# Kernel tuning notes

Hardware: AMD Instinct MI355X
Metric: run time of the kernel (lower is better)

The kernel has to match this reference:

```python
import jax, jax.numpy as jnp
import numpy as np

N = 50000
E = 1600000
D = 128
H = 16  # SE hidden = int(128 * 0.125)
EPS = 1e-5


def _layernorm(x, gamma, beta):
    mu = jnp.mean(x, axis=-1, keepdims=True)
    var = jnp.mean(jnp.square(x - mu), axis=-1, keepdims=True)
    return (x - mu) * jax.lax.rsqrt(var + EPS) * gamma + beta


def _gcn_conv(x, W, b, src, dst):
    # PyG GCNConv, improved=True: self-loop weight 2.0, symmetric norm.
    xw = x @ W                                        # [N, D]
    deg = jax.ops.segment_sum(jnp.ones((E,), x.dtype), dst, num_segments=N) + 2.0
    dinv = jnp.where(deg > 0, jax.lax.rsqrt(deg), 0.0)  # [N]
    norm = dinv[src] * dinv[dst]                      # [E]
    agg = jax.ops.segment_sum(xw[src] * norm[:, None], dst, num_segments=N)
    agg = agg + xw * (2.0 * dinv * dinv)[:, None]     # self-loop contribution
    return agg + b


def setup_inputs() -> dict:
    key = jax.random.key(0)
    ks = jax.random.split(key, 10)
    scale = 1.0 / np.sqrt(D)
    inp = {
        "x": jax.random.normal(ks[0], (N, D), jnp.float32),
        "edge_index": jax.random.randint(ks[1], (2, E), 0, N, jnp.int64),
        "W1": jax.random.normal(ks[2], (D, D), jnp.float32) * scale,
        "b1": jnp.zeros((D,), jnp.float32),
        "g1": jnp.ones((D,), jnp.float32),
        "beta1": jnp.zeros((D,), jnp.float32),
        "W2": jax.random.normal(ks[3], (D, D), jnp.float32) * scale,
        "b2": jnp.zeros((D,), jnp.float32),
        "g2": jnp.ones((D,), jnp.float32),
        "beta2": jnp.zeros((D,), jnp.float32),
        "Ws": jax.random.normal(ks[4], (D, H), jnp.float32) * scale,
        "bs": jnp.zeros((H,), jnp.float32),
        "We": jax.random.normal(ks[5], (H, D), jnp.float32) * (1.0 / np.sqrt(H)),
        "be": jnp.zeros((D,), jnp.float32),
    }
    return inp


def reference(x, edge_index, W1, b1, g1, beta1, W2, b2, g2, beta2, Ws, bs, We, be):
    src, dst = edge_index[0], edge_index[1]
    skip = x
    h = jax.nn.relu(_layernorm(_gcn_conv(x, W1, b1, src, dst), g1, beta1))
    h = _layernorm(_gcn_conv(h, W2, b2, src, dst), g2, beta2)
    # SE gating
    s = jax.nn.relu(h @ Ws + bs)
    w = jax.nn.sigmoid(s @ We + be)
    h = h * w
    return jax.nn.relu(h + skip)
```

## Files before the change

### kernel.cpp

```cpp
#include <hip/hip_runtime.h>
#include <math.h>

#define DD 128
#define HH 16
#define NB 256
#define TILE 8192
#define SEGCAP 24576
#define EPSV 1e-5f

typedef unsigned long long u64;
typedef __attribute__((ext_vector_type(8))) short short8;
typedef __attribute__((ext_vector_type(4))) float f32x4;
union U4S8 { uint4 u; short8 s; };

static __device__ __forceinline__ ushort f2bf(float f) {
  uint u = __float_as_uint(f);
  u += 0x7FFFu + ((u >> 16) & 1u);
  return (ushort)(u >> 16);
}
static __device__ __forceinline__ float bflo(uint u) { return __uint_as_float(u << 16); }
static __device__ __forceinline__ float bfhi(uint u) { return __uint_as_float(u & 0xFFFF0000u); }


__global__ void k_hist_cvt(const int* __restrict__ dst, int* __restrict__ deg, int ecnt,
                           const float2* __restrict__ x2, uint* __restrict__ xb,
                           int ncnt) {
  int stride = gridDim.x * blockDim.x;
  int t0 = blockIdx.x * blockDim.x + threadIdx.x;
  for (int e = t0; e < ecnt; e += stride) atomicAdd(&deg[dst[e]], 1);
  for (int k = t0; k < ncnt; k += stride) {
    float2 v = x2[k];
    xb[k] = (uint)f2bf(v.x) | ((uint)f2bf(v.y) << 16);
  }
}


#define SCAN_T 1024
#define SCAN_I 4

__global__ void k_scan1(const int* __restrict__ deg, u64* __restrict__ bsum, int n) {
  __shared__ u64 sh[SCAN_T];
  int tid = threadIdx.x;
  int base = blockIdx.x * SCAN_T * SCAN_I + tid * SCAN_I;
  u64 s = 0;
#pragma unroll
  for (int j = 0; j < SCAN_I; ++j) {
    int i = base + j;
    if (i < n) {
      int d = deg[i];
      int dp = (d + 7) & ~7;
      s += ((u64)dp << 32) | (u64)(uint)d;
    }
  }
  sh[tid] = s;
  __syncthreads();
  for (int off = SCAN_T / 2; off > 0; off >>= 1) {
    if (tid < off) sh[tid] += sh[tid + off];
    __syncthreads();
  }
  if (tid == 0) bsum[blockIdx.x] = sh[0];
}

__global__ void k_scan2(const int* __restrict__ deg, const u64* __restrict__ bsum,
                        int* __restrict__ rowoff, int* __restrict__ cursor,
                        int* __restrict__ bucketBase, int* __restrict__ bucketCur,
                        int n) {
  __shared__ u64 sh[SCAN_T];
  __shared__ u64 sbase;
  int tid = threadIdx.x;
  int b = blockIdx.x;
  if (tid == 0) { u64 s = 0; for (int j = 0; j < b; ++j) s += bsum[j]; sbase = s; }
  int base = b * SCAN_T * SCAN_I + tid * SCAN_I;
  int d[SCAN_I]; u64 ts = 0;
#pragma unroll
  for (int j = 0; j < SCAN_I; ++j) {
    int i = base + j;
    d[j] = (i < n) ? deg[i] : 0;
    int dp = (d[j] + 7) & ~7;
    ts += ((u64)dp << 32) | (u64)(uint)d[j];
  }
  sh[tid] = ts;
  __syncthreads();
  for (int off = 1; off < SCAN_T; off <<= 1) {
    u64 v = (tid >= off) ? sh[tid - off] : 0;
    __syncthreads();
    sh[tid] += v;
    __syncthreads();
  }
  u64 ex = sbase + sh[tid] - ts;
#pragma unroll
  for (int j = 0; j < SCAN_I; ++j) {
    int i = base + j;
    if (i < n) {
      int ro = (int)(ex >> 32);
      int raw = (int)(ex & 0xFFFFFFFFu);
      rowoff[i] = ro;
      cursor[i] = ro;
      int bq = (int)(((uint)i * NB) / (uint)n);
      if (i == (bq * n + NB - 1) / NB) { bucketBase[bq] = raw; bucketCur[bq] = raw; }
      int dp = (d[j] + 7) & ~7;
      ex += ((u64)dp << 32) | (u64)(uint)d[j];
      if (i == n - 1) rowoff[n] = (int)(ex >> 32);
    }
  }
}


static __device__ __forceinline__ void gemm_mfma_body(
    const uint4* __restrict__ A16, const float* __restrict__ B,
    const int* __restrict__ deg, ushort* __restrict__ C, int nrows, int bx) {
  int tid = threadIdx.x;
  int wv = tid >> 6, l = tid & 63;
  int rowbase = (bx >> 1) * 64;
  int c0 = (bx & 1) * 64;
  int colb = c0 + (wv << 4) + (l & 15);
  int kb = (l >> 4) << 3;
  uint4 bf[4];
#pragma unroll
  for (int ks = 0; ks < 4; ++ks) {
    const float* Bp = B + (size_t)(ks * 32 + kb) * DD + colb;
    float b0 = Bp[0], b1 = Bp[DD], b2 = Bp[2 * DD], b3 = Bp[3 * DD];
    float b4 = Bp[4 * DD], b5 = Bp[5 * DD], b6 = Bp[6 * DD], b7 = Bp[7 * DD];
    bf[ks].x = (uint)f2bf(b0) | ((uint)f2bf(b1) << 16);
    bf[ks].y = (uint)f2bf(b2) | ((uint)f2bf(b3) << 16);
    bf[ks].z = (uint)f2bf(b4) | ((uint)f2bf(b5) << 16);
    bf[ks].w = (uint)f2bf(b6) | ((uint)f2bf(b7) << 16);
  }
#pragma unroll
  for (int rt = 0; rt < 4; ++rt) {
    int r = rowbase + rt * 16 + (l & 15);
    int rc = (r < nrows) ? r : (nrows - 1);
    f32x4 acc = {0.f, 0.f, 0.f, 0.f};
#pragma unroll
    for (int ks = 0; ks < 4; ++ks) {
      U4S8 ua, ub;
      ua.u = A16[(size_t)rc * 16 + (ks << 2) + (l >> 4)];
      ub.u = bf[ks];
      acc = __builtin_amdgcn_mfma_f32_16x16x32_bf16(ua.s, ub.s, acc, 0, 0, 0);
    }
#pragma unroll
    for (int ri = 0; ri < 4; ++ri) {
      int row = rowbase + rt * 16 + ((l >> 4) << 2) + ri;
      if (row < nrows) {
        float dv = rsqrtf((float)deg[row] + 2.0f);
        C[(size_t)row * DD + colb] = f2bf(acc[ri] * dv);
      }
    }
  }
}


__global__ __launch_bounds__(256) void k_gemm1_bucket(
    const uint4* __restrict__ A16, const float* __restrict__ B,
    const int* __restrict__ deg, ushort* __restrict__ C, int nrows,
    const int* __restrict__ src, const int* __restrict__ dst,
    int* __restrict__ bucketCur, uint* __restrict__ pairs, int ecnt,
    int abloks, int gblocks) {
  __shared__ uint smem[8960];
  int bx = blockIdx.x;
  if (bx >= abloks) {
    gemm_mfma_body(A16, B, deg, C, nrows, bx - abloks);
    return;
  }
  uint* stag  = smem;
  uint* cnt   = smem + 8192;
  uint* gbase = smem + 8448;
  uint* cur   = smem + 8704;
  int tid = threadIdx.x;
  int ntiles = (ecnt + TILE - 1) / TILE;
  for (int t = bx; t < ntiles; t += abloks) {
    int base = t * TILE;
    int cntE = min(TILE, ecnt - base);
    cnt[tid] = 0;
    __syncthreads();
    for (int k = tid; k < cntE; k += 256) {
      uint d = (uint)dst[base + k];
      atomicAdd(&cnt[(d * NB) / (uint)nrows], 1u);
    }
    __syncthreads();
    uint myc = cnt[tid];
    uint gb = atomicAdd((uint*)&bucketCur[tid], myc);
    uint v = myc;
#pragma unroll
    for (int off = 1; off < 64; off <<= 1) {
      uint u = __shfl_up(v, off, 64);
      if ((tid & 63) >= off) v += u;
    }
    if ((tid & 63) == 63) gbase[tid >> 6] = v;
    __syncthreads();
    uint add = 0;
#pragma unroll
    for (int wvi = 0; wvi < 4; ++wvi) add += (wvi < (tid >> 6)) ? gbase[wvi] : 0;
    uint excl = add + v - myc;
    __syncthreads();
    cnt[tid] = excl;
    gbase[tid] = gb;
    cur[tid] = 0;
    __syncthreads();
    for (int k = tid; k < cntE; k += 256) {
      uint d = (uint)dst[base + k];
      uint s = (uint)src[base + k];
      uint b = (d * NB) / (uint)nrows;
      uint li = atomicAdd(&cur[b], 1u);
      stag[cnt[b] + li] = (d << 16) | s;
    }
    __syncthreads();
    int wv = tid >> 6, ln = tid & 63;
    for (int b = wv; b < 256; b += 4) {
      uint c = cur[b], o = cnt[b], g = gbase[b];
      for (uint k2 = (uint)ln; k2 < c; k2 += 64) pairs[g + k2] = stag[o + k2];
    }
    __syncthreads();
  }
}

__global__ __launch_bounds__(256) void k_gemmb(
    const uint4* __restrict__ A16, const float* __restrict__ B,
    const int* __restrict__ deg, ushort* __restrict__ C, int nrows) {
  gemm_mfma_body(A16, B, deg, C, nrows, blockIdx.x);
}


__global__ __launch_bounds__(256) void k_csrb(
    const uint* __restrict__ pairs, const int* __restrict__ bucketBase,
    const int* __restrict__ rowoff, const int* __restrict__ deg,
    int* __restrict__ cursor, ushort* __restrict__ csr, int n, int ecnt) {
  __shared__ ushort seg[SEGCAP];
  __shared__ int curs[256];
  int b = blockIdx.x;
  int tid = threadIdx.x;
  int d0 = (b * n + NB - 1) / NB;
  int d1 = ((b + 1) * n + NB - 1) / NB;
  int segbase = rowoff[d0];
  int seglen = rowoff[d1] - segbase;
  int pbase = bucketBase[b];
  int pend = (b == NB - 1) ? ecnt : bucketBase[b + 1];
  if (seglen <= SEGCAP) {
    for (int dl = tid; dl < d1 - d0; dl += 256) curs[dl] = rowoff[d0 + dl] - segbase;
    __syncthreads();
    for (int p = pbase + tid; p < pend; p += 256) {
      uint pr = pairs[p];
      int pos = atomicAdd(&curs[(int)(pr >> 16) - d0], 1);
      seg[pos] = (ushort)(pr & 0xFFFFu);
    }
    __syncthreads();
    for (int dl = tid; dl < d1 - d0; dl += 256) {
      int e0 = curs[dl], e1 = rowoff[d0 + dl + 1] - segbase;
      for (int k = e0; k < e1; ++k) seg[k] = (ushort)n;
    }
    __syncthreads();
    uint4* outp4 = (uint4*)(csr + segbase);
    const uint4* sp = (const uint4*)seg;
    int nq = seglen >> 3;
    for (int k = tid; k < nq; k += 256) outp4[k] = sp[k];
  } else {
    for (int p = pbase + tid; p < pend; p += 256) {
      uint pr = pairs[p];
      int pos = atomicAdd(&cursor[pr >> 16], 1);
      csr[pos] = (ushort)(pr & 0xFFFFu);
    }
    __syncthreads();
    for (int dl = tid; dl < d1 - d0; dl += 256) {
      int d = d0 + dl;
      for (int k = rowoff[d] + deg[d]; k < rowoff[d + 1]; ++k) csr[k] = (ushort)n;
    }
  }
}


static __device__ __forceinline__ void edge_accum(
    const uint* __restrict__ xw32, const ushort* __restrict__ csr,
    int start, int cnt, uint lane, float& acc0, float& acc1) {
  const uint4* cs = (const uint4*)(csr + __builtin_amdgcn_readfirstlane(start));
  int rem = __builtin_amdgcn_readfirstlane(cnt);
  uint4 c;
  if (rem >= 8) c = *cs++;
  while (rem >= 16) {
    uint v[8];
    v[0] = xw32[((c.x & 0xFFFFu) << 6) + lane];
    v[1] = xw32[((c.x >> 16) << 6) + lane];
    v[2] = xw32[((c.y & 0xFFFFu) << 6) + lane];
    v[3] = xw32[((c.y >> 16) << 6) + lane];
    v[4] = xw32[((c.z & 0xFFFFu) << 6) + lane];
    v[5] = xw32[((c.z >> 16) << 6) + lane];
    v[6] = xw32[((c.w & 0xFFFFu) << 6) + lane];
    v[7] = xw32[((c.w >> 16) << 6) + lane];
    uint4 cn = *cs++;
#pragma unroll
    for (int j = 0; j < 8; ++j) {
      acc0 += bflo(v[j]);
      acc1 += bfhi(v[j]);
    }
    c = cn; rem -= 8;
  }
  if (rem >= 8) {
    uint v[8];
    v[0] = xw32[((c.x & 0xFFFFu) << 6) + lane];
    v[1] = xw32[((c.x >> 16) << 6) + lane];
    v[2] = xw32[((c.y & 0xFFFFu) << 6) + lane];
    v[3] = xw32[((c.y >> 16) << 6) + lane];
    v[4] = xw32[((c.z & 0xFFFFu) << 6) + lane];
    v[5] = xw32[((c.z >> 16) << 6) + lane];
    v[6] = xw32[((c.w & 0xFFFFu) << 6) + lane];
    v[7] = xw32[((c.w >> 16) << 6) + lane];
#pragma unroll
    for (int j = 0; j < 8; ++j) {
      acc0 += bflo(v[j]);
      acc1 += bfhi(v[j]);
    }
  }
}


__global__ __launch_bounds__(256) void k_agg1(
    const ushort* __restrict__ xwd, const ushort* __restrict__ csr,
    const int* __restrict__ rowoff, const int* __restrict__ deg,
    const float* __restrict__ bias, const float* __restrict__ gam,
    const float* __restrict__ bet, uint* __restrict__ outp, int n) {
  int wv = threadIdx.x >> 6, lane = threadIdx.x & 63;
  int i = blockIdx.x * 4 + wv;
  if (i >= n) return;
  int start = rowoff[i], cnt = rowoff[i + 1] - start;
  float di = rsqrtf((float)deg[i] + 2.0f);
  const uint* xw32 = (const uint*)xwd;
  float acc0 = 0.f, acc1 = 0.f;
  edge_accum(xw32, csr, start, cnt, (uint)lane, acc0, acc1);
  uint su = xw32[((uint)i << 6) + lane];
  float2 bv = ((const float2*)bias)[lane];
  float c0v = fmaf(di, acc0 + 2.f * bflo(su), bv.x);
  float c1v = fmaf(di, acc1 + 2.f * bfhi(su), bv.y);
  float s = c0v + c1v;
#pragma unroll
  for (int off = 32; off > 0; off >>= 1) s += __shfl_xor(s, off);
  float mu = s * (1.f / DD);
  float c0 = c0v - mu, c1 = c1v - mu;
  float q = c0 * c0 + c1 * c1;
#pragma unroll
  for (int off = 32; off > 0; off >>= 1) q += __shfl_xor(q, off);
  float rstd = rsqrtf(q * (1.f / DD) + EPSV);
  float2 gv = ((const float2*)gam)[lane];
  float2 tv = ((const float2*)bet)[lane];
  float h0 = fmaxf(fmaf(c0 * rstd, gv.x, tv.x), 0.f);
  float h1 = fmaxf(fmaf(c1 * rstd, gv.y, tv.y), 0.f);
  uint packed = (uint)f2bf(h0) | ((uint)f2bf(h1) << 16);
  __builtin_nontemporal_store(packed, &outp[((uint)i << 6) + lane]);
}


__global__ __launch_bounds__(256) void k_agg2(
    const ushort* __restrict__ xwd, const ushort* __restrict__ csr,
    const int* __restrict__ rowoff, const int* __restrict__ deg,
    const float* __restrict__ bias, const float* __restrict__ gam,
    const float* __restrict__ bet, const float* __restrict__ Ws,
    const float* __restrict__ bs, const float* __restrict__ We,
    const float* __restrict__ be, const float* __restrict__ xin,
    float* __restrict__ outp, int n) {
  int wv = threadIdx.x >> 6, lane = threadIdx.x & 63;
  int i = blockIdx.x * 4 + wv;
  if (i >= n) return;
  int start = rowoff[i], cnt = rowoff[i + 1] - start;
  float di = rsqrtf((float)deg[i] + 2.0f);
  const uint* xw32 = (const uint*)xwd;
  float acc0 = 0.f, acc1 = 0.f;
  edge_accum(xw32, csr, start, cnt, (uint)lane, acc0, acc1);
  uint su = xw32[((uint)i << 6) + lane];
  float2 bv = ((const float2*)bias)[lane];
  float c0v = fmaf(di, acc0 + 2.f * bflo(su), bv.x);
  float c1v = fmaf(di, acc1 + 2.f * bfhi(su), bv.y);
  float s = c0v + c1v;
#pragma unroll
  for (int off = 32; off > 0; off >>= 1) s += __shfl_xor(s, off);
  float mu = s * (1.f / DD);
  float c0 = c0v - mu, c1 = c1v - mu;
  float q = c0 * c0 + c1 * c1;
#pragma unroll
  for (int off = 32; off > 0; off >>= 1) q += __shfl_xor(q, off);
  float rstd = rsqrtf(q * (1.f / DD) + EPSV);
  float2 gv = ((const float2*)gam)[lane];
  float2 tv = ((const float2*)bet)[lane];
  float h0 = fmaf(c0 * rstd, gv.x, tv.x);
  float h1 = fmaf(c1 * rstd, gv.y, tv.y);
  float pj[HH];
  const float* wr0 = &Ws[(2 * lane) * HH];
  const float* wr1 = &Ws[(2 * lane + 1) * HH];
#pragma unroll
  for (int j = 0; j < HH; ++j) pj[j] = h0 * wr0[j] + h1 * wr1[j];
#pragma unroll
  for (int off = 32; off > 0; off >>= 1) {
#pragma unroll
    for (int j = 0; j < HH; ++j) pj[j] += __shfl_xor(pj[j], off);
  }
  float2 bev = ((const float2*)be)[lane];
  float wacc0 = bev.x, wacc1 = bev.y;
#pragma unroll
  for (int j = 0; j < HH; ++j) {
    float sj = fmaxf(pj[j] + bs[j], 0.f);
    float2 wev = ((const float2*)(We + j * DD))[lane];
    wacc0 = fmaf(sj, wev.x, wacc0);
    wacc1 = fmaf(sj, wev.y, wacc1);
  }
  float w0 = 1.f / (1.f + __expf(-wacc0));
  float w1 = 1.f / (1.f + __expf(-wacc1));
  float2 xr = ((const float2*)(xin + (size_t)i * DD))[lane];
  float2 o;
  o.x = fmaxf(fmaf(h0, w0, xr.x), 0.f);
  o.y = fmaxf(fmaf(h1, w1, xr.y), 0.f);
  ((float2*)(outp + (size_t)i * DD))[lane] = o;
}


extern "C" void kernel_launch(void* const* d_in, const int* in_sizes, int n_in,
                              void* d_out, int out_size, void* d_ws, size_t ws_size,
                              hipStream_t stream) {
  const float* x   = (const float*)d_in[0];
  const int*   ei  = (const int*)d_in[1];
  const float* W1  = (const float*)d_in[2];
  const float* b1  = (const float*)d_in[3];
  const float* g1  = (const float*)d_in[4];
  const float* be1 = (const float*)d_in[5];
  const float* W2  = (const float*)d_in[6];
  const float* b2  = (const float*)d_in[7];
  const float* g2  = (const float*)d_in[8];
  const float* be2 = (const float*)d_in[9];
  const float* Ws  = (const float*)d_in[10];
  const float* bs  = (const float*)d_in[11];
  const float* We  = (const float*)d_in[12];
  const float* bee = (const float*)d_in[13];
  float* outp = (float*)d_out;

  int n    = in_sizes[0] / DD;
  int ecnt = in_sizes[1] / 2;
  const int* src = ei;
  const int* dst = ei + ecnt;

  size_t maxent = (size_t)ecnt + 8 * (size_t)n + 64;

  char* w = (char*)d_ws;
  ushort* xwd    = (ushort*)w; w += (size_t)(n + 1) * DD * 2;
  uint*   h1     = (uint*)w;   w += (size_t)n * DD * 2;
  uint*   xb     = (uint*)w;   w += (size_t)n * DD * 2;
  int*    deg    = (int*)w;    w += (size_t)n * 4;
  int*    cursor = (int*)w;    w += (size_t)n * 4;
  int*    rowoff = (int*)w;    w += (size_t)(n + 1) * 4;
  w = (char*)(((size_t)w + 7) & ~(size_t)7);
  u64*    bsum   = (u64*)w;    w += 64 * 8;
  int*    bktB   = (int*)w;    w += NB * 4;
  int*    bktC   = (int*)w;    w += NB * 4;
  w = (char*)(((size_t)w + 15) & ~(size_t)15);
  uint*   pairs  = (uint*)w;   w += ((size_t)ecnt + 64) * 4;
  w = (char*)(((size_t)w + 15) & ~(size_t)15);
  ushort* csr    = (ushort*)w; w += maxent * 2;

  hipMemsetAsync(deg, 0, (size_t)n * 4, stream);
  hipMemsetAsync(xwd + (size_t)n * DD, 0, DD * 2, stream);

  const int TB = 256;
  k_hist_cvt<<<2048, TB, 0, stream>>>(dst, deg, ecnt, (const float2*)x, xb, n * 64);
  int nb = (n + SCAN_T * SCAN_I - 1) / (SCAN_T * SCAN_I);
  k_scan1<<<nb, SCAN_T, 0, stream>>>(deg, bsum, n);
  k_scan2<<<nb, SCAN_T, 0, stream>>>(deg, bsum, rowoff, cursor, bktB, bktC, n);

  int gblocks = ((n + 63) / 64) * 2;
  int abloks = (ecnt + TILE - 1) / TILE;
  k_gemm1_bucket<<<abloks + gblocks, TB, 0, stream>>>(
      (const uint4*)xb, W1, deg, xwd, n, src, dst, bktC, pairs, ecnt, abloks, gblocks);
  k_csrb<<<NB, TB, 0, stream>>>(pairs, bktB, rowoff, deg, cursor, csr, n, ecnt);

  int nb4 = (n + 3) / 4;
  k_agg1<<<nb4, TB, 0, stream>>>(xwd, csr, rowoff, deg, b1, g1, be1, h1, n);
  k_gemmb<<<gblocks, TB, 0, stream>>>((const uint4*)h1, W2, deg, xwd, n);
  k_agg2<<<nb4, TB, 0, stream>>>(xwd, csr, rowoff, deg, b2, g2, be2,
                                 Ws, bs, We, bee, x, outp, n);
}
```

Measured before the change: 310.9 us.

## Fuse second GEMM into first aggregation and pre-pack weights into MFMA fragments

The layer-1 aggregation kernel now keeps each block's four normalized rows in shared memory as bf16. It multiplies them by a pre-packed W2 with MFMA and writes the scaled second-layer features directly. This removes the h1 intermediate buffer's store and reload and the separate second GEMM launch. The first GEMM now reads fp32 x and converts to bf16 inline, which drops the standalone x conversion pass. Both weight matrices are packed once into MFMA fragment layout inside the histogram kernel. In exchange, the fused MFMA uses only 4 of its 16 rows, so most of that compute is wasted, and it adds a block-wide barrier.

```diff
diff --git a/kernel.cpp b/kernel.cpp
--- a/kernel.cpp
+++ b/kernel.cpp
@@ -18,19 +18,32 @@
   u += 0x7FFFu + ((u >> 16) & 1u);
   return (ushort)(u >> 16);
 }
+static __device__ __forceinline__ uint pk(float a, float b) {
+  return (uint)f2bf(a) | ((uint)f2bf(b) << 16);
+}
 static __device__ __forceinline__ float bflo(uint u) { return __uint_as_float(u << 16); }
 static __device__ __forceinline__ float bfhi(uint u) { return __uint_as_float(u & 0xFFFF0000u); }
 
 
-__global__ void k_hist_cvt(const int* __restrict__ dst, int* __restrict__ deg, int ecnt,
-                           const float2* __restrict__ x2, uint* __restrict__ xb,
-                           int ncnt) {
+__global__ void k_hist_prep(const int* __restrict__ dst, int* __restrict__ deg, int ecnt,
+                            const float* __restrict__ W1, const float* __restrict__ W2,
+                            uint4* __restrict__ W1f, uint4* __restrict__ W2f) {
   int stride = gridDim.x * blockDim.x;
   int t0 = blockIdx.x * blockDim.x + threadIdx.x;
   for (int e = t0; e < ecnt; e += stride) atomicAdd(&deg[dst[e]], 1);
-  for (int k = t0; k < ncnt; k += stride) {
-    float2 v = x2[k];
-    xb[k] = (uint)f2bf(v.x) | ((uint)f2bf(v.y) << 16);
+  for (int t = t0; t < 4096; t += stride) {
+    int m = t >> 11;
+    int r = t & 2047;
+    int ct = r >> 8, ks = (r >> 6) & 3, l = r & 63;
+    int col = ct * 16 + (l & 15);
+    int kb = ks * 32 + ((l >> 4) << 3);
+    const float* W = m ? W2 : W1;
+    uint4 v;
+    v.x = pk(W[(kb + 0) * DD + col], W[(kb + 1) * DD + col]);
+    v.y = pk(W[(kb + 2) * DD + col], W[(kb + 3) * DD + col]);
+    v.z = pk(W[(kb + 4) * DD + col], W[(kb + 5) * DD + col]);
+    v.w = pk(W[(kb + 6) * DD + col], W[(kb + 7) * DD + col]);
+    (m ? W2f : W1f)[(ct * 4 + ks) * 64 + l] = v;
   }
 }
 
@@ -106,26 +119,17 @@
 }
 
 
-static __device__ __forceinline__ void gemm_mfma_body(
-    const uint4* __restrict__ A16, const float* __restrict__ B,
+static __device__ __forceinline__ void gemm_mfma_x(
+    const float* __restrict__ x, const uint4* __restrict__ W1f,
     const int* __restrict__ deg, ushort* __restrict__ C, int nrows, int bx) {
   int tid = threadIdx.x;
   int wv = tid >> 6, l = tid & 63;
   int rowbase = (bx >> 1) * 64;
-  int c0 = (bx & 1) * 64;
-  int colb = c0 + (wv << 4) + (l & 15);
-  int kb = (l >> 4) << 3;
+  int ctg = (bx & 1) * 4 + wv;
+  int colb = ctg * 16 + (l & 15);
   uint4 bf[4];
 #pragma unroll
-  for (int ks = 0; ks < 4; ++ks) {
-    const float* Bp = B + (size_t)(ks * 32 + kb) * DD + colb;
-    float b0 = Bp[0], b1 = Bp[DD], b2 = Bp[2 * DD], b3 = Bp[3 * DD];
-    float b4 = Bp[4 * DD], b5 = Bp[5 * DD], b6 = Bp[6 * DD], b7 = Bp[7 * DD];
-    bf[ks].x = (uint)f2bf(b0) | ((uint)f2bf(b1) << 16);
-    bf[ks].y = (uint)f2bf(b2) | ((uint)f2bf(b3) << 16);
-    bf[ks].z = (uint)f2bf(b4) | ((uint)f2bf(b5) << 16);
-    bf[ks].w = (uint)f2bf(b6) | ((uint)f2bf(b7) << 16);
-  }
+  for (int ks = 0; ks < 4; ++ks) bf[ks] = W1f[(ctg * 4 + ks) * 64 + l];
 #pragma unroll
   for (int rt = 0; rt < 4; ++rt) {
     int r = rowbase + rt * 16 + (l & 15);
@@ -133,8 +137,13 @@
     f32x4 acc = {0.f, 0.f, 0.f, 0.f};
 #pragma unroll
     for (int ks = 0; ks < 4; ++ks) {
+      const float4* xp = (const float4*)(x + (size_t)rc * DD + ks * 32 + ((l >> 4) << 3));
+      float4 a0 = xp[0], a1 = xp[1];
       U4S8 ua, ub;
-      ua.u = A16[(size_t)rc * 16 + (ks << 2) + (l >> 4)];
+      ua.u.x = pk(a0.x, a0.y);
+      ua.u.y = pk(a0.z, a0.w);
+      ua.u.z = pk(a1.x, a1.y);
+      ua.u.w = pk(a1.z, a1.w);
       ub.u = bf[ks];
       acc = __builtin_amdgcn_mfma_f32_16x16x32_bf16(ua.s, ub.s, acc, 0, 0, 0);
     }
@@ -151,7 +160,7 @@
 
 
 __global__ __launch_bounds__(256) void k_gemm1_bucket(
-    const uint4* __restrict__ A16, const float* __restrict__ B,
+    const float* __restrict__ x, const uint4* __restrict__ W1f,
     const int* __restrict__ deg, ushort* __restrict__ C, int nrows,
     const int* __restrict__ src, const int* __restrict__ dst,
     int* __restrict__ bucketCur, uint* __restrict__ pairs, int ecnt,
@@ -159,7 +168,7 @@
   __shared__ uint smem[8960];
   int bx = blockIdx.x;
   if (bx >= abloks) {
-    gemm_mfma_body(A16, B, deg, C, nrows, bx - abloks);
+    gemm_mfma_x(x, W1f, deg, C, nrows, bx - abloks);
     return;
   }
   uint* stag  = smem;
@@ -212,12 +221,6 @@
     }
     __syncthreads();
   }
-}
-
-__global__ __launch_bounds__(256) void k_gemmb(
-    const uint4* __restrict__ A16, const float* __restrict__ B,
-    const int* __restrict__ deg, ushort* __restrict__ C, int nrows) {
-  gemm_mfma_body(A16, B, deg, C, nrows, blockIdx.x);
 }
 
 
@@ -312,20 +315,23 @@
 }
 
 
-__global__ __launch_bounds__(256) void k_agg1(
+__global__ __launch_bounds__(256) void k_agg1f(
     const ushort* __restrict__ xwd, const ushort* __restrict__ csr,
     const int* __restrict__ rowoff, const int* __restrict__ deg,
     const float* __restrict__ bias, const float* __restrict__ gam,
-    const float* __restrict__ bet, uint* __restrict__ outp, int n) {
+    const float* __restrict__ bet, const uint4* __restrict__ W2f,
+    ushort* __restrict__ xwd2, int n) {
+  __shared__ uint hls[16 * 64];
+  __shared__ float dvs[4];
   int wv = threadIdx.x >> 6, lane = threadIdx.x & 63;
   int i = blockIdx.x * 4 + wv;
-  if (i >= n) return;
-  int start = rowoff[i], cnt = rowoff[i + 1] - start;
-  float di = rsqrtf((float)deg[i] + 2.0f);
+  int iv = (i < n) ? i : (n - 1);
+  int start = rowoff[iv], cnt = rowoff[iv + 1] - start;
+  float di = rsqrtf((float)deg[iv] + 2.0f);
   const uint* xw32 = (const uint*)xwd;
   float acc0 = 0.f, acc1 = 0.f;
   edge_accum(xw32, csr, start, cnt, (uint)lane, acc0, acc1);
-  uint su = xw32[((uint)i << 6) + lane];
+  uint su = xw32[((uint)iv << 6) + lane];
   float2 bv = ((const float2*)bias)[lane];
   float c0v = fmaf(di, acc0 + 2.f * bflo(su), bv.x);
   float c1v = fmaf(di, acc1 + 2.f * bfhi(su), bv.y);
@@ -342,8 +348,29 @@
   float2 tv = ((const float2*)bet)[lane];
   float h0 = fmaxf(fmaf(c0 * rstd, gv.x, tv.x), 0.f);
   float h1 = fmaxf(fmaf(c1 * rstd, gv.y, tv.y), 0.f);
-  uint packed = (uint)f2bf(h0) | ((uint)f2bf(h1) << 16);
-  __builtin_nontemporal_store(packed, &outp[((uint)i << 6) + lane]);
+  hls[wv * 64 + lane] = pk(h0, h1);
+  if (lane == 0) dvs[wv] = di;
+  __syncthreads();
+#pragma unroll
+  for (int cti = 0; cti < 2; ++cti) {
+    int ct = wv * 2 + cti;
+    f32x4 acc = {0.f, 0.f, 0.f, 0.f};
+#pragma unroll
+    for (int ks = 0; ks < 4; ++ks) {
+      U4S8 ua, ub;
+      ua.u = *(const uint4*)&hls[(lane & 15) * 64 + ks * 16 + ((lane >> 4) << 2)];
+      ub.u = W2f[(ct * 4 + ks) * 64 + lane];
+      acc = __builtin_amdgcn_mfma_f32_16x16x32_bf16(ua.s, ub.s, acc, 0, 0, 0);
+    }
+    if (lane < 16) {
+#pragma unroll
+      for (int ri = 0; ri < 4; ++ri) {
+        int node = blockIdx.x * 4 + ri;
+        if (node < n)
+          xwd2[(size_t)node * DD + ct * 16 + lane] = f2bf(acc[ri] * dvs[ri]);
+      }
+    }
+  }
 }
 
 
@@ -437,12 +464,13 @@
 
   char* w = (char*)d_ws;
   ushort* xwd    = (ushort*)w; w += (size_t)(n + 1) * DD * 2;
-  uint*   h1     = (uint*)w;   w += (size_t)n * DD * 2;
-  uint*   xb     = (uint*)w;   w += (size_t)n * DD * 2;
+  ushort* xwd2   = (ushort*)w; w += (size_t)(n + 1) * DD * 2;
   int*    deg    = (int*)w;    w += (size_t)n * 4;
   int*    cursor = (int*)w;    w += (size_t)n * 4;
   int*    rowoff = (int*)w;    w += (size_t)(n + 1) * 4;
-  w = (char*)(((size_t)w + 7) & ~(size_t)7);
+  w = (char*)(((size_t)w + 15) & ~(size_t)15);
+  uint4*  W1f    = (uint4*)w;  w += 2048 * 16;
+  uint4*  W2f    = (uint4*)w;  w += 2048 * 16;
   u64*    bsum   = (u64*)w;    w += 64 * 8;
   int*    bktB   = (int*)w;    w += NB * 4;
   int*    bktC   = (int*)w;    w += NB * 4;
@@ -453,9 +481,10 @@
 
   hipMemsetAsync(deg, 0, (size_t)n * 4, stream);
   hipMemsetAsync(xwd + (size_t)n * DD, 0, DD * 2, stream);
+  hipMemsetAsync(xwd2 + (size_t)n * DD, 0, DD * 2, stream);
 
   const int TB = 256;
-  k_hist_cvt<<<2048, TB, 0, stream>>>(dst, deg, ecnt, (const float2*)x, xb, n * 64);
+  k_hist_prep<<<2048, TB, 0, stream>>>(dst, deg, ecnt, W1, W2, W1f, W2f);
   int nb = (n + SCAN_T * SCAN_I - 1) / (SCAN_T * SCAN_I);
   k_scan1<<<nb, SCAN_T, 0, stream>>>(deg, bsum, n);
   k_scan2<<<nb, SCAN_T, 0, stream>>>(deg, bsum, rowoff, cursor, bktB, bktC, n);
@@ -463,12 +492,11 @@
   int gblocks = ((n + 63) / 64) * 2;
   int abloks = (ecnt + TILE - 1) / TILE;
   k_gemm1_bucket<<<abloks + gblocks, TB, 0, stream>>>(
-      (const uint4*)xb, W1, deg, xwd, n, src, dst, bktC, pairs, ecnt, abloks, gblocks);
+      x, W1f, deg, xwd, n, src, dst, bktC, pairs, ecnt, abloks, gblocks);
   k_csrb<<<NB, TB, 0, stream>>>(pairs, bktB, rowoff, deg, cursor, csr, n, ecnt);
 
   int nb4 = (n + 3) / 4;
-  k_agg1<<<nb4, TB, 0, stream>>>(xwd, csr, rowoff, deg, b1, g1, be1, h1, n);
-  k_gemmb<<<gblocks, TB, 0, stream>>>((const uint4*)h1, W2, deg, xwd, n);
-  k_agg2<<<nb4, TB, 0, stream>>>(xwd, csr, rowoff, deg, b2, g2, be2,
+  k_agg1f<<<nb4, TB, 0, stream>>>(xwd, csr, rowoff, deg, b1, g1, be1, W2f, xwd2, n);
+  k_agg2<<<nb4, TB, 0, stream>>>(xwd2, csr, rowoff, deg, b2, g2, be2,
                                  Ws, bs, We, bee, x, outp, n);
 }
```

Measured after the change: 306.1 us. Within noise of the previous version (-1.6%).
